# Kernel optimization log

Measured on AMD Instinct MI355X. Metric: run time of the kernel, lower is better.

Reference implementation:

```python
import jax, jax.numpy as jnp
import numpy as np

S, B, D, H, DH = 1024, 4, 1024, 16, 64


def setup_inputs() -> dict:
    key = jax.random.key(0)
    ks = jax.random.split(key, 12)
    inp = {
        "query": jax.random.normal(ks[0], (S, B, D), dtype=jnp.float32),
        "key": jax.random.normal(ks[1], (S, B, D), dtype=jnp.float32),
        "value": jax.random.normal(ks[2], (S, B, D), dtype=jnp.float32),
        "key_mask": jax.random.randint(ks[3], (S, B), 0, 2, dtype=jnp.int32),
        # per-head stacked projection weights (original loops nn.Linear per head)
        "Wq": jax.random.normal(ks[4], (H, D, DH), dtype=jnp.float32) * 0.02,
        "bq": jnp.zeros((H, DH), dtype=jnp.float32),
        "Wk": jax.random.normal(ks[5], (H, D, DH), dtype=jnp.float32) * 0.02,
        "bk": jnp.zeros((H, DH), dtype=jnp.float32),
        "Wv": jax.random.normal(ks[6], (H, D, DH), dtype=jnp.float32) * 0.02,
        "bv": jnp.zeros((H, DH), dtype=jnp.float32),
        "Wo": jax.random.normal(ks[7], (H * DH, D), dtype=jnp.float32) * 0.02,
        "bo": jnp.zeros((D,), dtype=jnp.float32),
    }
    return inp


def reference(query, key, value, key_mask, Wq, bq, Wk, bk, Wv, bv, Wo, bo):
    # query/key/value: [S, B, D] (seq-major, matching torch einsum 'imk,jmk->imj')
    q = jnp.einsum('smd,hdk->smhk', query, Wq) + bq  # [Sq, B, H, DH]
    k = jnp.einsum('smd,hdk->smhk', key, Wk) + bk    # [Sk, B, H, DH]
    v = jnp.einsum('smd,hdk->smhk', value, Wv) + bv  # [Sk, B, H, DH]

    scale = 1.0 / jnp.sqrt(jnp.float32(DH))
    scores = jnp.einsum('imhk,jmhk->himj', q, k) * scale  # [H, Sq, B, Sk]
    # key_mask: [Sk, B] -> transpose -> [B, Sk]; additive -1e18 masking
    scores = scores - key_mask.astype(jnp.float32).T * 1e18
    attn = jax.nn.softmax(scores, axis=-1)
    out = jnp.einsum('himj,jmhk->imhk', attn, v)  # [Sq, B, H, DH]
    concat = out.reshape(out.shape[0], out.shape[1], H * DH)
    return concat @ Wo + bo  # [Sq, B, D]
```

## Files before the change

### kernel.cpp

```cpp
#include <hip/hip_runtime.h>
#include <hip/hip_bf16.h>


typedef __attribute__((ext_vector_type(8))) short short8;
typedef __attribute__((ext_vector_type(4))) short short4_;
typedef __attribute__((ext_vector_type(4))) float f32x4;
typedef __attribute__((ext_vector_type(16))) float f32x16;
typedef __attribute__((ext_vector_type(8))) __bf16 bf16x8;
typedef __attribute__((ext_vector_type(4))) __bf16 bf16x4;

union B8 {
    short8 s;
    bf16x8 b;
    unsigned short u[8];
};
union B4 {
    short4_ s;
    bf16x4 b;
    unsigned short u[4];
    int i[2];
};

#if __has_builtin(__builtin_amdgcn_exp2f)
#define EXP2(x) __builtin_amdgcn_exp2f(x)
#else
#define EXP2(x) exp2f(x)
#endif
#if __has_builtin(__builtin_amdgcn_rcpf)
#define RCP(x) __builtin_amdgcn_rcpf(x)
#else
#define RCP(x) (1.0f / (x))
#endif

static __device__ __forceinline__ unsigned short f2bf_rne(float f) {
    union { float f; unsigned u; } v; v.f = f;
    unsigned r = v.u + 0x7FFFu + ((v.u >> 16) & 1u);
    return (unsigned short)(r >> 16);
}

static __device__ __forceinline__ void async_lds16(const void* g, const void* l) {
    __builtin_amdgcn_global_load_lds(
        (const __attribute__((address_space(1))) unsigned int*)(unsigned long long)g,
        (__attribute__((address_space(3))) unsigned int*)(unsigned int)(unsigned long long)l,
        16, 0, 0);
}

__global__ __launch_bounds__(256) void prep(
    const float* __restrict__ Wq, const float* __restrict__ Wk,
    const float* __restrict__ Wv, const float* __restrict__ Wo,
    const float* __restrict__ query, const float* __restrict__ key,
    const float* __restrict__ value,
    unsigned short* __restrict__ WT,
    unsigned short* __restrict__ qA, unsigned short* __restrict__ kA,
    unsigned short* __restrict__ vA) {
    const int t = threadIdx.x;
    const int z = blockIdx.z;

    if (z >= 4) {
        const int zz = z - 4;
        const int tensor = zz >> 2;
        const int part = zz & 3;
        const float* src = (tensor == 0) ? query : (tensor == 1) ? key : value;
        unsigned short* dst = (tensor == 0) ? qA : (tensor == 1) ? kA : vA;
        const int blk = blockIdx.y * 16 + blockIdx.x;
        const size_t base = (size_t)part * 1048576 + (size_t)blk * 4096 + t * 16;
        B8 w0, w1;
#pragma unroll
        for (int i = 0; i < 2; ++i) {
            f32x4 a = *(const f32x4*)(src + base + i * 8);
            f32x4 b = *(const f32x4*)(src + base + i * 8 + 4);
#pragma unroll
            for (int j = 0; j < 4; ++j) {
                (i ? w1 : w0).u[j] = f2bf_rne(a[j]);
                (i ? w1 : w0).u[4 + j] = f2bf_rne(b[j]);
            }
        }
        *(short8*)(dst + base) = w0.s;
        *(short8*)(dst + base + 8) = w1.s;
        return;
    }

    __shared__ float sT[64][65];
    const int dtile = blockIdx.x;
    const int sub = blockIdx.y;
    const float* src;
    int spitch;
    unsigned short* dst;
    if (z < 3) {
        const float* W = (z == 0) ? Wq : (z == 1) ? Wk : Wv;
        src = W + (size_t)sub * 65536 + (size_t)dtile * 64 * 64;
        spitch = 64;
        dst = WT + (size_t)z * 1048576 + (size_t)(sub * 64) * 1024 + dtile * 64;
    } else {
        src = Wo + (size_t)dtile * 64 * 1024 + sub * 64;
        spitch = 1024;
        dst = WT + (size_t)3 * 1048576 + (size_t)(sub * 64) * 1024 + dtile * 64;
    }

    const int r = t >> 2;
    const int cseg = (t & 3) * 16;
#pragma unroll
    for (int i = 0; i < 4; ++i) {
        f32x4 v = *(const f32x4*)(src + (size_t)r * spitch + cseg + i * 4);
#pragma unroll
        for (int j = 0; j < 4; ++j) sT[r][cseg + i * 4 + j] = v[j];
    }
    __syncthreads();
    B8 w0, w1;
#pragma unroll
    for (int i = 0; i < 8; ++i) {
        w0.u[i] = f2bf_rne(sT[cseg + i][r]);
        w1.u[i] = f2bf_rne(sT[cseg + 8 + i][r]);
    }
    *(short8*)(dst + (size_t)r * 1024 + cseg) = w0.s;
    *(short8*)(dst + (size_t)r * 1024 + cseg + 8) = w1.s;
}

template <bool OUT_F32, bool BIAS_ROW>
__device__ __forceinline__ void gemm128(unsigned short* __restrict__ sA,
                                        unsigned short* __restrict__ sB,
                                        const unsigned short* __restrict__ A,
                                        size_t lda,
                                        const unsigned short* __restrict__ Bt,
                                        size_t ldb,
                                        const float* __restrict__ bias,
                                        void* __restrict__ Cv, size_t ldc,
                                        float oscale, int row0, int col0) {
    const int t = threadIdx.x;
    const int w = t >> 6;
    const int lane = t & 63;
    const int quad = lane >> 4;
    const int l15 = lane & 15;
    const int wr = w >> 1;
    const int wc = w & 1;
    const int srow16 = lane >> 2;
    const int sgseg = (lane & 3) ^ ((lane >> 3) & 3);
    const int rseg = (quad ^ ((l15 >> 1) & 3)) * 8;

    f32x4 acc[4][4] = {};

    const unsigned short* agp = A + (size_t)(row0 + w * 32 + srow16) * lda + sgseg * 8;
    const unsigned short* agp2 = agp + (size_t)16 * lda;
    const unsigned short* bgp = Bt + (size_t)(col0 + w * 32 + srow16) * ldb + sgseg * 8;
    const unsigned short* bgp2 = bgp + (size_t)16 * ldb;
    const int ldsA0 = (w * 32) * 32;
    const int ldsA1 = (w * 32 + 16) * 32;

    async_lds16(agp, sA + ldsA0);
    async_lds16(agp2, sA + ldsA1);
    async_lds16(bgp, sB + ldsA0);
    async_lds16(bgp2, sB + ldsA1);

#pragma unroll 2
    for (int tt = 0; tt < 32; ++tt) {
        const int cur = tt & 1;
        __syncthreads();
        if (tt < 31) {
            const int nb = cur ^ 1;
            const int k0 = (tt + 1) * 32;
            async_lds16(agp + k0, sA + nb * 4096 + ldsA0);
            async_lds16(agp2 + k0, sA + nb * 4096 + ldsA1);
            async_lds16(bgp + k0, sB + nb * 4096 + ldsA0);
            async_lds16(bgp2 + k0, sB + nb * 4096 + ldsA1);
        }
        const unsigned short* sac = sA + cur * 4096;
        const unsigned short* sbc = sB + cur * 4096;
        B8 af[4], bf[4];
#pragma unroll
        for (int i = 0; i < 4; ++i)
            af[i].s = *(const short8*)&sac[(wr * 64 + i * 16 + l15) * 32 + rseg];
#pragma unroll
        for (int j = 0; j < 4; ++j)
            bf[j].s = *(const short8*)&sbc[(wc * 64 + j * 16 + l15) * 32 + rseg];
#pragma unroll
        for (int i = 0; i < 4; ++i)
#pragma unroll
            for (int j = 0; j < 4; ++j)
                acc[i][j] = __builtin_amdgcn_mfma_f32_16x16x32_bf16(af[i].b, bf[j].b,
                                                                    acc[i][j], 0, 0, 0);
    }

    float brow[4][4];
    if constexpr (BIAS_ROW) {
#pragma unroll
        for (int i = 0; i < 4; ++i)
#pragma unroll
            for (int r = 0; r < 4; ++r)
                brow[i][r] = bias[row0 + wr * 64 + i * 16 + quad * 4 + r];
    }
#pragma unroll
    for (int j = 0; j < 4; ++j) {
        const int col = col0 + wc * 64 + j * 16 + l15;
        const float bcol = BIAS_ROW ? 0.0f : bias[col];
#pragma unroll
        for (int i = 0; i < 4; ++i) {
#pragma unroll
            for (int r = 0; r < 4; ++r) {
                const int row = row0 + wr * 64 + i * 16 + quad * 4 + r;
                const size_t idx = (size_t)row * ldc + col;
                const float bb = BIAS_ROW ? brow[i][r] : bcol;
                const float val = (acc[i][j][r] + bb) * oscale;
                if constexpr (OUT_F32)
                    ((float*)Cv)[idx] = val;
                else
                    ((unsigned short*)Cv)[idx] = f2bf_rne(val);
            }
        }
    }
}

#define SCALE_L2E 0.18033688011112042f

__global__ __launch_bounds__(256) void qkv_gemm(
    const unsigned short* __restrict__ qA, const unsigned short* __restrict__ kA,
    const unsigned short* __restrict__ vA,
    const unsigned short* __restrict__ WT,
    const float* __restrict__ bq, const float* __restrict__ bk, const float* __restrict__ bv,
    unsigned short* q_o, unsigned short* k_o, unsigned short* vT_o) {
    __shared__ unsigned short sA[2 * 128 * 32];
    __shared__ unsigned short sB[2 * 128 * 32];
    const int p = blockIdx.z;
    if (p < 2) {
        const unsigned short* A = (p == 0) ? qA : kA;
        const unsigned short* Bt = WT + (size_t)p * 1048576;
        const float* bias = (p == 0) ? bq : bk;
        unsigned short* C = (p == 0) ? q_o : k_o;
        const float osc = (p == 0) ? SCALE_L2E : 1.0f;
        gemm128<false, false>(sA, sB, A, 1024, Bt, 1024, bias, C, 1024, osc,
                              blockIdx.x * 128, blockIdx.y * 128);
    } else {
        const int b = blockIdx.x >> 3;
        const int rt = blockIdx.x & 7;
        gemm128<false, true>(sA, sB, WT + (size_t)2 * 1048576, 1024,
                             vA + (size_t)b * 1024, 4096, bv,
                             vT_o + (size_t)b * 1048576, 1024, 1.0f,
                             rt * 128, blockIdx.y * 128);
    }
}

__global__ __launch_bounds__(256) void out_gemm(const unsigned short* __restrict__ A,
                                                const unsigned short* __restrict__ WT,
                                                const float* __restrict__ bo,
                                                float* __restrict__ C) {
    __shared__ unsigned short sA[2 * 128 * 32];
    __shared__ unsigned short sB[2 * 128 * 32];
    gemm128<true, false>(sA, sB, A, 1024, WT + (size_t)3 * 1048576, 1024, bo, C, 1024,
                         1.0f, blockIdx.x * 128, blockIdx.y * 128);
}

#define TP 72

#if __has_builtin(__builtin_amdgcn_mfma_f32_32x32x8bf16_1k)
#define HAVE_X8 1
#endif

__global__ __launch_bounds__(256) void attn_kernel(
    const unsigned short* __restrict__ q,
    const unsigned short* __restrict__ k,
    const unsigned short* __restrict__ vT,
    const int* __restrict__ key_mask,
    unsigned short* __restrict__ o) {
    __shared__ unsigned short sK[2][64 * TP];
    __shared__ unsigned short sVt[2][64 * TP];
    __shared__ float sBias[1024];
    __shared__ unsigned long long sBits[16];

    const int t = threadIdx.x;
    const int wave = t >> 6;
    const int lane = t & 63;
    const int n31 = lane & 31;
    const int hh = lane >> 5;

    const int L = blockIdx.x + 8 * (blockIdx.y + 4 * blockIdx.z);
    const int xcd = L & 7;
    const int kk = L >> 3;
    const int g = (xcd << 3) | (kk >> 3);
    const int qt = kk & 7;
    const int b = g & 3;
    const int h = g >> 2;
    const int q0w = qt * 128 + wave * 32;

    const int srow = t >> 3;
    const int sseg = t & 7;

#pragma unroll
    for (int i = 0; i < 4; ++i) {
        const int idx = i * 4 + wave;
        const int sk = idx * 64 + lane;
        unsigned long long bal = __ballot(key_mask[sk * 4 + b] != 0);
        if (lane == 0) sBits[idx] = bal;
    }
    __syncthreads();
#pragma unroll
    for (int i = 0; i < 4; ++i) {
        const int idx = t * 4 + i;
        const int r = idx & 15;
        const int hb = (idx >> 4) & 1;
        const int blk = (idx >> 5) & 1;
        const int kt = idx >> 6;
        const int row = (r & 3) + 8 * (r >> 2) + 4 * hb + blk * 32;
        sBias[idx] = ((sBits[kt] >> row) & 1ull) ? -16384.0f : 0.0f;
    }

    bf16x8 qf[4];
    {
        const unsigned short* qrow =
            q + ((size_t)(q0w + n31) * 4 + b) * 1024 + h * 64 + hh * 8;
#pragma unroll
        for (int kc = 0; kc < 4; ++kc) {
            B8 tmp;
            tmp.s = *(const short8*)(qrow + kc * 16);
            qf[kc] = tmp.b;
        }
    }

    f32x16 O0 = {}, O1 = {}, L_ = {};
    B4 ones;
#pragma unroll
    for (int j = 0; j < 4; ++j) ones.u[j] = 0x3F80;
#if !defined(HAVE_X8)
    B8 ones8;
#pragma unroll
    for (int j = 0; j < 8; ++j) ones8.u[j] = 0x3F80;
#endif

    const unsigned short* kbase = k + (size_t)b * 1024 + h * 64;
    const unsigned short* vtb = vT + ((size_t)(b * 16 + h) * 64) * 1024;

    {
        const unsigned short* kr = kbase + (size_t)srow * 4096 + sseg * 8;
        short8 ka = *(const short8*)kr;
        short8 kb2 = *(const short8*)(kr + (size_t)32 * 4096);
        const unsigned short* vr = vtb + (size_t)srow * 1024 + sseg * 8;
        short8 va = *(const short8*)vr;
        short8 vb2 = *(const short8*)(vr + (size_t)32 * 1024);
        *(short8*)&sK[0][srow * TP + sseg * 8] = ka;
        *(short8*)&sK[0][(32 + srow) * TP + sseg * 8] = kb2;
        *(short8*)&sVt[0][srow * TP + sseg * 8] = va;
        *(short8*)&sVt[0][(32 + srow) * TP + sseg * 8] = vb2;
    }

#pragma unroll 2
    for (int kt = 0; kt < 16; ++kt) {
        const int cur = kt & 1;
        __syncthreads();
        short8 nka, nkb, nva, nvb;
        if (kt < 15) {
            const int k0n = (kt + 1) * 64;
            const unsigned short* kr = kbase + (size_t)(k0n + srow) * 4096 + sseg * 8;
            nka = *(const short8*)kr;
            nkb = *(const short8*)(kr + (size_t)32 * 4096);
            const unsigned short* vr = vtb + (size_t)srow * 1024 + k0n + sseg * 8;
            nva = *(const short8*)vr;
            nvb = *(const short8*)(vr + (size_t)32 * 1024);
        }
        B4 pfr[2][4];
#pragma unroll
        for (int blk = 0; blk < 2; ++blk) {
            f32x16 c;
            const f32x4* bp = (const f32x4*)&sBias[((kt * 2 + blk) * 2 + hh) * 16];
#pragma unroll
            for (int i = 0; i < 4; ++i) {
                f32x4 x = bp[i];
#pragma unroll
                for (int j = 0; j < 4; ++j) c[i * 4 + j] = x[j];
            }
            __builtin_amdgcn_s_setprio(1);
#pragma unroll
            for (int kc = 0; kc < 4; ++kc) {
                B8 af;
                af.s = *(const short8*)&sK[cur][(blk * 32 + n31) * TP + kc * 16 + hh * 8];
                c = __builtin_amdgcn_mfma_f32_32x32x16_bf16(af.b, qf[kc], c, 0, 0, 0);
            }
            __builtin_amdgcn_s_setprio(0);
#pragma unroll
            for (int gg = 0; gg < 4; ++gg)
#pragma unroll
                for (int j = 0; j < 4; ++j)
                    pfr[blk][gg].b[j] = (__bf16)EXP2(c[gg * 4 + j]);
        }
#if defined(HAVE_X8)
        __builtin_amdgcn_s_setprio(1);
#pragma unroll
        for (int blk = 0; blk < 2; ++blk) {
#pragma unroll
            for (int gg = 0; gg < 4; ++gg) {
                const int sko = blk * 32 + gg * 8 + hh * 4;
                B4 b0, b1;
                b0.s = *(const short4_*)&sVt[cur][n31 * TP + sko];
                b1.s = *(const short4_*)&sVt[cur][(32 + n31) * TP + sko];
                O0 = __builtin_amdgcn_mfma_f32_32x32x8bf16_1k(pfr[blk][gg].s, b0.s, O0, 0, 0, 0);
                O1 = __builtin_amdgcn_mfma_f32_32x32x8bf16_1k(pfr[blk][gg].s, b1.s, O1, 0, 0, 0);
                L_ = __builtin_amdgcn_mfma_f32_32x32x8bf16_1k(pfr[blk][gg].s, ones.s, L_, 0, 0, 0);
            }
        }
        __builtin_amdgcn_s_setprio(0);
#else
        __builtin_amdgcn_s_setprio(1);
#pragma unroll
        for (int blk = 0; blk < 2; ++blk) {
            B4 par[4];
#pragma unroll
            for (int gg = 0; gg < 4; ++gg) {
                par[gg].i[0] = __shfl_xor(pfr[blk][gg].i[0], 32);
                par[gg].i[1] = __shfl_xor(pfr[blk][gg].i[1], 32);
            }
#pragma unroll
            for (int w = 0; w < 2; ++w) {
                const int gsel = 2 * w + hh;
                B4 lo = (hh == 0) ? pfr[blk][gsel] : par[gsel];
                B4 hi = (hh == 0) ? par[gsel] : pfr[blk][gsel];
                B8 afr;
#pragma unroll
                for (int j = 0; j < 4; ++j) {
                    afr.u[j] = lo.u[j];
                    afr.u[4 + j] = hi.u[j];
                }
                const int sko = blk * 32 + w * 16 + hh * 8;
                B8 b0, b1;
                b0.s = *(const short8*)&sVt[cur][n31 * TP + sko];
                b1.s = *(const short8*)&sVt[cur][(32 + n31) * TP + sko];
                O0 = __builtin_amdgcn_mfma_f32_32x32x16_bf16(afr.b, b0.b, O0, 0, 0, 0);
                O1 = __builtin_amdgcn_mfma_f32_32x32x16_bf16(afr.b, b1.b, O1, 0, 0, 0);
                L_ = __builtin_amdgcn_mfma_f32_32x32x16_bf16(afr.b, ones8.b, L_, 0, 0, 0);
            }
        }
        __builtin_amdgcn_s_setprio(0);
#endif
        if (kt < 15) {
            const int nb = 1 - cur;
            *(short8*)&sK[nb][srow * TP + sseg * 8] = nka;
            *(short8*)&sK[nb][(32 + srow) * TP + sseg * 8] = nkb;
            *(short8*)&sVt[nb][srow * TP + sseg * 8] = nva;
            *(short8*)&sVt[nb][(32 + srow) * TP + sseg * 8] = nvb;
        }
    }

    unsigned short* obase = o + ((size_t)q0w * 4 + b) * 1024 + h * 64 + n31;
#pragma unroll
    for (int r = 0; r < 16; ++r) {
        const int qr = (r & 3) + 8 * (r >> 2) + 4 * hh;
        const float inv = RCP(L_[r]);
        obase[(size_t)qr * 4096] = f2bf_rne(O0[r] * inv);
        obase[(size_t)qr * 4096 + 32] = f2bf_rne(O1[r] * inv);
    }
}

extern "C" void kernel_launch(void* const* d_in, const int* in_sizes, int n_in,
                              void* d_out, int out_size, void* d_ws, size_t ws_size,
                              hipStream_t stream) {
    const float* query = (const float*)d_in[0];
    const float* key_ = (const float*)d_in[1];
    const float* value = (const float*)d_in[2];
    const int* key_mask = (const int*)d_in[3];
    const float* Wq = (const float*)d_in[4];
    const float* bq = (const float*)d_in[5];
    const float* Wk = (const float*)d_in[6];
    const float* bk = (const float*)d_in[7];
    const float* Wv = (const float*)d_in[8];
    const float* bv = (const float*)d_in[9];
    const float* Wo = (const float*)d_in[10];
    const float* bo = (const float*)d_in[11];
    float* out = (float*)d_out;

    const size_t NE = (size_t)4096 * 1024;
    unsigned short* q_ws = (unsigned short*)d_ws;
    unsigned short* k_ws = q_ws + NE;
    unsigned short* v_ws = k_ws + NE;
    unsigned short* a_ws = v_ws + NE;
    unsigned short* wt_ws = a_ws + NE;

    unsigned short* qA = a_ws;
    unsigned short* kA = (unsigned short*)d_out;
    unsigned short* vA = kA + NE;

    prep<<<dim3(16, 16, 16), 256, 0, stream>>>(Wq, Wk, Wv, Wo, query, key_, value,
                                               wt_ws, qA, kA, vA);
    qkv_gemm<<<dim3(32, 8, 3), 256, 0, stream>>>(qA, kA, vA, wt_ws,
                                                 bq, bk, bv, q_ws, k_ws, v_ws);
    attn_kernel<<<dim3(8, 4, 16), 256, 0, stream>>>(q_ws, k_ws, v_ws, key_mask, a_ws);
    out_gemm<<<dim3(32, 8, 1), 256, 0, stream>>>(a_ws, wt_ws, bo, out);
}
```

Measured before the change: 213.9 us.

## Triple-buffer GEMM LDS staging with explicit vmcnt waits and barriers

Replaces the double-buffered async global-to-LDS loop in the shared 128x128 GEMM with a three-stage ring buffer, issuing loads two tiles ahead. Uses explicit s_waitcnt vmcnt(4) plus a raw s_barrier instead of __syncthreads, so one tile's loads can stay in flight while the next is consumed. The aim is to hide global memory latency behind MFMA work, at the cost of 50% more LDS per block, which may lower occupancy.

```diff
diff --git a/kernel.cpp b/kernel.cpp
--- a/kernel.cpp
+++ b/kernel.cpp
@@ -146,25 +146,16 @@
     const int ldsA0 = (w * 32) * 32;
     const int ldsA1 = (w * 32 + 16) * 32;
 
-    async_lds16(agp, sA + ldsA0);
-    async_lds16(agp2, sA + ldsA1);
-    async_lds16(bgp, sB + ldsA0);
-    async_lds16(bgp2, sB + ldsA1);
-
-#pragma unroll 2
-    for (int tt = 0; tt < 32; ++tt) {
-        const int cur = tt & 1;
-        __syncthreads();
-        if (tt < 31) {
-            const int nb = cur ^ 1;
-            const int k0 = (tt + 1) * 32;
-            async_lds16(agp + k0, sA + nb * 4096 + ldsA0);
-            async_lds16(agp2 + k0, sA + nb * 4096 + ldsA1);
-            async_lds16(bgp + k0, sB + nb * 4096 + ldsA0);
-            async_lds16(bgp2 + k0, sB + nb * 4096 + ldsA1);
-        }
-        const unsigned short* sac = sA + cur * 4096;
-        const unsigned short* sbc = sB + cur * 4096;
+    auto STAGE = [&](int tt, int off) {
+        const int k0 = tt * 32;
+        async_lds16(agp + k0, sA + off + ldsA0);
+        async_lds16(agp2 + k0, sA + off + ldsA1);
+        async_lds16(bgp + k0, sB + off + ldsA0);
+        async_lds16(bgp2 + k0, sB + off + ldsA1);
+    };
+    auto COMPUTE = [&](int off) {
+        const unsigned short* sac = sA + off;
+        const unsigned short* sbc = sB + off;
         B8 af[4], bf[4];
 #pragma unroll
         for (int i = 0; i < 4; ++i)
@@ -178,7 +169,31 @@
             for (int j = 0; j < 4; ++j)
                 acc[i][j] = __builtin_amdgcn_mfma_f32_16x16x32_bf16(af[i].b, bf[j].b,
                                                                     acc[i][j], 0, 0, 0);
-    }
+    };
+
+    STAGE(0, 0);
+    STAGE(1, 4096);
+
+    for (int t3 = 0; t3 < 30; t3 += 3) {
+        asm volatile("s_waitcnt vmcnt(4)" ::: "memory");
+        __builtin_amdgcn_s_barrier();
+        STAGE(t3 + 2, 8192);
+        COMPUTE(0);
+        asm volatile("s_waitcnt vmcnt(4)" ::: "memory");
+        __builtin_amdgcn_s_barrier();
+        STAGE(t3 + 3, 0);
+        COMPUTE(4096);
+        asm volatile("s_waitcnt vmcnt(4)" ::: "memory");
+        __builtin_amdgcn_s_barrier();
+        STAGE(t3 + 4, 4096);
+        COMPUTE(8192);
+    }
+    asm volatile("s_waitcnt vmcnt(4)" ::: "memory");
+    __builtin_amdgcn_s_barrier();
+    COMPUTE(0);
+    asm volatile("s_waitcnt vmcnt(0)" ::: "memory");
+    __builtin_amdgcn_s_barrier();
+    COMPUTE(4096);
 
     float brow[4][4];
     if constexpr (BIAS_ROW) {
@@ -217,8 +232,8 @@
     const unsigned short* __restrict__ WT,
     const float* __restrict__ bq, const float* __restrict__ bk, const float* __restrict__ bv,
     unsigned short* q_o, unsigned short* k_o, unsigned short* vT_o) {
-    __shared__ unsigned short sA[2 * 128 * 32];
-    __shared__ unsigned short sB[2 * 128 * 32];
+    __shared__ unsigned short sA[3 * 128 * 32];
+    __shared__ unsigned short sB[3 * 128 * 32];
     const int p = blockIdx.z;
     if (p < 2) {
         const unsigned short* A = (p == 0) ? qA : kA;
@@ -242,8 +257,8 @@
                                                 const unsigned short* __restrict__ WT,
                                                 const float* __restrict__ bo,
                                                 float* __restrict__ C) {
-    __shared__ unsigned short sA[2 * 128 * 32];
-    __shared__ unsigned short sB[2 * 128 * 32];
+    __shared__ unsigned short sA[3 * 128 * 32];
+    __shared__ unsigned short sB[3 * 128 * 32];
     gemm128<true, false>(sA, sB, A, 1024, WT + (size_t)3 * 1048576, 1024, bo, C, 1024,
                          1.0f, blockIdx.x * 128, blockIdx.y * 128);
 }
```

Result: faster. 199.9 us (-6.5%).
